# Optimization experiments

Measured on AMD Instinct MI355X. Metric: run time of the kernel, lower is better.

## Reference

```python
import jax, jax.numpy as jnp
import numpy as np

HEAD_SIZE = 64
EMB_SIZE = 1024
B, N = 4, 4096


def setup_inputs() -> dict:
    key = jax.random.key(0)
    kx, kk, kq, kv = jax.random.split(key, 4)
    x = jax.random.normal(kx, (B, N, EMB_SIZE), dtype=jnp.float32)
    # nn.Linear(emb, head, bias=False): weight [head, emb]; y = x @ W.T
    s = 1.0 / np.sqrt(EMB_SIZE)
    Wk = jax.random.uniform(kk, (HEAD_SIZE, EMB_SIZE), jnp.float32, -s, s)
    Wq = jax.random.uniform(kq, (HEAD_SIZE, EMB_SIZE), jnp.float32, -s, s)
    Wv = jax.random.uniform(kv, (HEAD_SIZE, EMB_SIZE), jnp.float32, -s, s)
    return {"x": x, "Wk": Wk, "Wq": Wq, "Wv": Wv}


def reference(x, Wk, Wq, Wv):
    # k, q, v: [B, N, H]
    k = jnp.einsum("bne,he->bnh", x, Wk)
    q = jnp.einsum("bne,he->bnh", x, Wq)
    v = jnp.einsum("bne,he->bnh", x, Wv)
    scale = HEAD_SIZE ** -0.5
    aff = jnp.einsum("bqh,bkh->bqk", q, k) * scale  # [B, N, N]
    aff = jax.nn.softmax(aff, axis=2)
    # dropout rate is 0.0 -> identity
    return jnp.einsum("bqk,bkh->bqh", aff, v)
```

## Files before the change

### kernel.cpp

```cpp
#include <hip/hip_runtime.h>

#define NB   4
#define SEQ  4096
#define EMB  1024
#define HS   64

typedef __attribute__((ext_vector_type(8))) short bf16x8;
typedef __attribute__((ext_vector_type(4))) float f32x4;

__device__ inline unsigned short f2bf(float f) {
  unsigned int u = __float_as_uint(f);
  u += 0x7fffu + ((u >> 16) & 1u);
  return (unsigned short)(u >> 16);
}
__device__ inline float bf2f(unsigned short h) {
  return __uint_as_float(((unsigned int)h) << 16);
}
__device__ inline int swzi64(int row, int c) {
  return row * 64 + ((c ^ (row & 7)) << 3);
}
__device__ inline int swzi32(int row, int c) {
  return row * 32 + ((c ^ ((row >> 1) & 3)) << 3);
}
__device__ inline int swzi128(int row, int c) {
  return row * 128 + ((c ^ (row & 7)) << 3);
}
__device__ inline void gld16(const unsigned short* g, unsigned short* l) {
  __builtin_amdgcn_global_load_lds(
      (const __attribute__((address_space(1))) void*)g,
      (__attribute__((address_space(3))) void*)l, 16, 0, 0);
}

__global__ __launch_bounds__(256) void wprep(
    const float* __restrict__ Wk, const float* __restrict__ Wq,
    const float* __restrict__ Wv,
    unsigned short* __restrict__ Wh, unsigned short* __restrict__ Wl) {
  int i = blockIdx.x * 256 + threadIdx.x;
  int e = i >> 8, c = i & 255;
  float4 v;
  float sc = 1.0f;
  if (e < 64)       { v = ((const float4*)Wq)[e * 256 + c];
                      sc = 0.18033688011112042f; }
  else if (e < 128)   v = ((const float4*)Wk)[(e - 64) * 256 + c];
  else                v = ((const float4*)Wv)[(e - 128) * 256 + c];
  v.x *= sc; v.y *= sc; v.z *= sc; v.w *= sc;
  ushort4 hv, lv;
  hv.x = f2bf(v.x); lv.x = f2bf(v.x - bf2f(hv.x));
  hv.y = f2bf(v.y); lv.y = f2bf(v.y - bf2f(hv.y));
  hv.z = f2bf(v.z); lv.z = f2bf(v.z - bf2f(hv.z));
  hv.w = f2bf(v.w); lv.w = f2bf(v.w - bf2f(hv.w));
  *(ushort4*)&Wh[i * 4] = hv;
  *(ushort4*)&Wl[i * 4] = lv;
}

#define XhSp(p) ((unsigned short*)(SM + (p) * 2048))
#define XlSp(p) ((unsigned short*)(SM + 4096 + (p) * 2048))
#define WhSp(p) ((unsigned short*)(SM + 8192 + (p) * 12288))
#define WlSp(p) ((unsigned short*)(SM + 32768 + (p) * 12288))

__global__ __launch_bounds__(256) void qkv_x1(
    const float* __restrict__ x,
    const unsigned short* __restrict__ Wh, const unsigned short* __restrict__ Wl,
    unsigned short* __restrict__ qh, unsigned short* __restrict__ ql,
    unsigned short* __restrict__ kh, unsigned short* __restrict__ kl,
    unsigned short* __restrict__ vt) {
  __shared__ __align__(16) unsigned char SM[57344];

  const int t  = threadIdx.x;
  const int l  = t & 63;
  const int li = l & 15;
  const int g  = l >> 4;
  const int w  = t >> 6;
  const int m0 = blockIdx.x * 32;
  const int b  = m0 >> 12;
  const int n0 = m0 & 4095;

  const int xrow = t >> 3;
  const float* xp = x + (m0 + xrow) * EMB + (t & 7) * 4;
  const int xaddr = xrow * 32 + ((((t & 7) >> 1) ^ ((xrow >> 1) & 3)) << 3)
                    + (t & 1) * 4;

  const int wconst = (l >> 2) * EMB + (((l & 3) ^ ((l >> 3) & 3)) << 3);

  f32x4 acc[2][3];
#pragma unroll
  for (int i = 0; i < 2; ++i)
#pragma unroll
    for (int j = 0; j < 3; ++j) acc[i][j] = (f32x4){0.f, 0.f, 0.f, 0.f};

  const int rA0 = li, rA1 = 16 + li;
  const int rB0 = 48 * w + li, rB1 = rB0 + 16, rB2 = rB0 + 32;

  auto issueW = [&](int s, int p) {
    const int ko = s * 32;
#pragma unroll
    for (int i = 0; i < 3; ++i) {
      const int seg = 3 * w + i;
      gld16(Wh + 16 * seg * EMB + wconst + ko, WhSp(p) + seg * 512);
      gld16(Wl + 16 * seg * EMB + wconst + ko, WlSp(p) + seg * 512);
    }
  };
  auto writeX = [&](float4 v, int p) {
    unsigned short h0 = f2bf(v.x), h1 = f2bf(v.y), h2 = f2bf(v.z), h3 = f2bf(v.w);
    unsigned short e0 = f2bf(v.x - bf2f(h0)), e1 = f2bf(v.y - bf2f(h1));
    unsigned short e2 = f2bf(v.z - bf2f(h2)), e3 = f2bf(v.w - bf2f(h3));
    int2 hv, lv;
    hv.x = (int)((unsigned)h0 | ((unsigned)h1 << 16));
    hv.y = (int)((unsigned)h2 | ((unsigned)h3 << 16));
    lv.x = (int)((unsigned)e0 | ((unsigned)e1 << 16));
    lv.y = (int)((unsigned)e2 | ((unsigned)e3 << 16));
    *(int2*)&XhSp(p)[xaddr] = hv;
    *(int2*)&XlSp(p)[xaddr] = lv;
  };

  float4 px = *(const float4*)xp;
  issueW(0, 0);
  writeX(px, 0);
  px = *(const float4*)(xp + 32);
  __syncthreads();

  for (int s = 0; s < 32; ++s) {
    const int p = s & 1;
    if (s < 31) {
      issueW(s + 1, p ^ 1);
      writeX(px, p ^ 1);
      if (s < 30) px = *(const float4*)(xp + (s + 2) * 32);
    }

    bf16x8 ah0 = *(const bf16x8*)&XhSp(p)[swzi32(rA0, g)];
    bf16x8 ah1 = *(const bf16x8*)&XhSp(p)[swzi32(rA1, g)];
    bf16x8 al0 = *(const bf16x8*)&XlSp(p)[swzi32(rA0, g)];
    bf16x8 al1 = *(const bf16x8*)&XlSp(p)[swzi32(rA1, g)];
    bf16x8 bh0 = *(const bf16x8*)&WhSp(p)[swzi32(rB0, g)];
    bf16x8 bh1 = *(const bf16x8*)&WhSp(p)[swzi32(rB1, g)];
    bf16x8 bh2 = *(const bf16x8*)&WhSp(p)[swzi32(rB2, g)];
    bf16x8 bl0 = *(const bf16x8*)&WlSp(p)[swzi32(rB0, g)];
    bf16x8 bl1 = *(const bf16x8*)&WlSp(p)[swzi32(rB1, g)];
    bf16x8 bl2 = *(const bf16x8*)&WlSp(p)[swzi32(rB2, g)];

    acc[0][0] = __builtin_amdgcn_mfma_f32_16x16x32_bf16(ah0, bh0, acc[0][0], 0,0,0);
    acc[0][0] = __builtin_amdgcn_mfma_f32_16x16x32_bf16(ah0, bl0, acc[0][0], 0,0,0);
    acc[0][0] = __builtin_amdgcn_mfma_f32_16x16x32_bf16(al0, bh0, acc[0][0], 0,0,0);
    acc[0][1] = __builtin_amdgcn_mfma_f32_16x16x32_bf16(ah0, bh1, acc[0][1], 0,0,0);
    acc[0][1] = __builtin_amdgcn_mfma_f32_16x16x32_bf16(ah0, bl1, acc[0][1], 0,0,0);
    acc[0][1] = __builtin_amdgcn_mfma_f32_16x16x32_bf16(al0, bh1, acc[0][1], 0,0,0);
    acc[0][2] = __builtin_amdgcn_mfma_f32_16x16x32_bf16(ah0, bh2, acc[0][2], 0,0,0);
    acc[0][2] = __builtin_amdgcn_mfma_f32_16x16x32_bf16(ah0, bl2, acc[0][2], 0,0,0);
    acc[0][2] = __builtin_amdgcn_mfma_f32_16x16x32_bf16(al0, bh2, acc[0][2], 0,0,0);
    acc[1][0] = __builtin_amdgcn_mfma_f32_16x16x32_bf16(ah1, bh0, acc[1][0], 0,0,0);
    acc[1][0] = __builtin_amdgcn_mfma_f32_16x16x32_bf16(ah1, bl0, acc[1][0], 0,0,0);
    acc[1][0] = __builtin_amdgcn_mfma_f32_16x16x32_bf16(al1, bh0, acc[1][0], 0,0,0);
    acc[1][1] = __builtin_amdgcn_mfma_f32_16x16x32_bf16(ah1, bh1, acc[1][1], 0,0,0);
    acc[1][1] = __builtin_amdgcn_mfma_f32_16x16x32_bf16(ah1, bl1, acc[1][1], 0,0,0);
    acc[1][1] = __builtin_amdgcn_mfma_f32_16x16x32_bf16(al1, bh1, acc[1][1], 0,0,0);
    acc[1][2] = __builtin_amdgcn_mfma_f32_16x16x32_bf16(ah1, bh2, acc[1][2], 0,0,0);
    acc[1][2] = __builtin_amdgcn_mfma_f32_16x16x32_bf16(ah1, bl2, acc[1][2], 0,0,0);
    acc[1][2] = __builtin_amdgcn_mfma_f32_16x16x32_bf16(al1, bh2, acc[1][2], 0,0,0);

    __syncthreads();
  }

#pragma unroll
  for (int i = 0; i < 2; ++i)
#pragma unroll
    for (int j = 0; j < 3; ++j) {
      const int H3 = 48 * w + 16 * j + li;
#pragma unroll
      for (int r = 0; r < 4; ++r) {
        const int mrow = 16 * i + 4 * g + r;
        const float vv = acc[i][j][r];
        if (H3 < 64) {
          const unsigned short hb = f2bf(vv);
          const int off = (b * SEQ + n0 + mrow) * HS + H3;
          qh[off] = hb; ql[off] = f2bf(vv - bf2f(hb));
        } else if (H3 < 128) {
          const unsigned short hb = f2bf(vv);
          const int off = (b * SEQ + n0 + mrow) * HS + (H3 - 64);
          kh[off] = hb; kl[off] = f2bf(vv - bf2f(hb));
        } else {
          vt[(b * HS + (H3 - 128)) * SEQ + n0 + mrow] = f2bf(vv);
        }
      }
    }
}

__global__ __launch_bounds__(512) void attn_mfma(
    const unsigned short* __restrict__ qh, const unsigned short* __restrict__ ql,
    const unsigned short* __restrict__ kh, const unsigned short* __restrict__ kl,
    const unsigned short* __restrict__ vt, float* __restrict__ out) {
  __shared__ __align__(16) unsigned char SM[69632];
  unsigned short* const KhS = (unsigned short*)SM;
  unsigned short* const KlS = (unsigned short*)(SM + 16384);
  unsigned short* const VtS = (unsigned short*)(SM + 32768);
  unsigned short* const PtS = (unsigned short*)(SM + 49152);

  const int t  = threadIdx.x;
  const int l  = t & 63;
  const int li = l & 15;
  const int g  = l >> 4;
  const int w  = t >> 6;
  const int qg = w & 1;
  const int ks = w >> 1;
  const int b  = blockIdx.y;
  const int q0 = blockIdx.x << 6;

  bf16x8 qfh[2][2], qfl[2][2];
#pragma unroll
  for (int qs = 0; qs < 2; ++qs) {
    const unsigned short* qrh = qh + (b * SEQ + q0 + 32 * qg + 16 * qs + li) * HS;
    const unsigned short* qrl = ql + (b * SEQ + q0 + 32 * qg + 16 * qs + li) * HS;
    qfh[qs][0] = *(const bf16x8*)&qrh[8 * g];
    qfh[qs][1] = *(const bf16x8*)&qrh[32 + 8 * g];
    qfl[qs][0] = *(const bf16x8*)&qrl[8 * g];
    qfl[qs][1] = *(const bf16x8*)&qrl[32 + 8 * g];
  }

  const int kconst = (l >> 3) * HS + (((l & 7) ^ (l >> 3)) << 3);
  const int rowl = l >> 4, slot = l & 15;
  const int vcE = rowl * SEQ + ((slot ^ rowl) << 3);
  const int vcO = rowl * SEQ + ((slot ^ (4 + rowl)) << 3);
  const unsigned short* khB = kh + b * SEQ * HS;
  const unsigned short* klB = kl + b * SEQ * HS;
  const unsigned short* vtB = vt + b * HS * SEQ;
  const int sA = 2 * w, sB = 2 * w + 1;

  f32x4 O[4][2];
#pragma unroll
  for (int ht = 0; ht < 4; ++ht) {
    O[ht][0] = (f32x4){0.f, 0.f, 0.f, 0.f};
    O[ht][1] = (f32x4){0.f, 0.f, 0.f, 0.f};
  }
  float lp0 = 0.f, lp1 = 0.f;
  unsigned short* const PtW = PtS + w * 1280;

  for (int it = 0; it < 32; ++it) {
    const int kt0 = it << 7;
    __syncthreads();
    gld16(khB + (kt0 + 8 * sA) * HS + kconst, KhS + sA * 512);
    gld16(khB + (kt0 + 8 * sB) * HS + kconst, KhS + sB * 512);
    gld16(klB + (kt0 + 8 * sA) * HS + kconst, KlS + sA * 512);
    gld16(klB + (kt0 + 8 * sB) * HS + kconst, KlS + sB * 512);
    gld16(vtB + 4 * sA * SEQ + kt0 + vcE, VtS + sA * 512);
    gld16(vtB + 4 * sB * SEQ + kt0 + vcO, VtS + sB * 512);
    __syncthreads();

    f32x4 S[2][2];
    S[0][0] = (f32x4){-32.f, -32.f, -32.f, -32.f};
    S[0][1] = (f32x4){-32.f, -32.f, -32.f, -32.f};
    S[1][0] = (f32x4){-32.f, -32.f, -32.f, -32.f};
    S[1][1] = (f32x4){-32.f, -32.f, -32.f, -32.f};
#pragma unroll
    for (int khf = 0; khf < 2; ++khf) {
      const int cc = 4 * khf + g;
#pragma unroll
      for (int kt = 0; kt < 2; ++kt) {
        const int row = 32 * ks + 16 * kt + li;
        bf16x8 akh = *(const bf16x8*)&KhS[swzi64(row, cc)];
        bf16x8 akl = *(const bf16x8*)&KlS[swzi64(row, cc)];
        S[kt][0] = __builtin_amdgcn_mfma_f32_16x16x32_bf16(akh, qfh[0][khf], S[kt][0], 0,0,0);
        S[kt][0] = __builtin_amdgcn_mfma_f32_16x16x32_bf16(akh, qfl[0][khf], S[kt][0], 0,0,0);
        S[kt][0] = __builtin_amdgcn_mfma_f32_16x16x32_bf16(akl, qfh[0][khf], S[kt][0], 0,0,0);
        S[kt][1] = __builtin_amdgcn_mfma_f32_16x16x32_bf16(akh, qfh[1][khf], S[kt][1], 0,0,0);
        S[kt][1] = __builtin_amdgcn_mfma_f32_16x16x32_bf16(akh, qfl[1][khf], S[kt][1], 0,0,0);
        S[kt][1] = __builtin_amdgcn_mfma_f32_16x16x32_bf16(akl, qfh[1][khf], S[kt][1], 0,0,0);
      }
    }

#pragma unroll
    for (int kt = 0; kt < 2; ++kt)
#pragma unroll
      for (int qs = 0; qs < 2; ++qs) {
        unsigned pu[4];
        float ls = 0.f;
#pragma unroll
        for (int r = 0; r < 4; ++r) {
          const float pe = exp2f(S[kt][qs][r]);
          pu[r] = __float_as_uint(pe);
          ls += __uint_as_float(pu[r] & 0xffff0000u);
        }
        if (qs == 0) lp0 += ls; else lp1 += ls;
        const unsigned p01 = __builtin_amdgcn_perm(pu[1], pu[0], 0x07060302u);
        const unsigned p23 = __builtin_amdgcn_perm(pu[3], pu[2], 0x07060302u);
        const int qrow = 16 * qs + li;
        const int c = 2 * kt + (g >> 1);
        const int addr = qrow * 40 + (((c ^ (qrow & 3))) << 3) + ((g & 1) << 2);
        int2 pv; pv.x = (int)p01; pv.y = (int)p23;
        *(int2*)&PtW[addr] = pv;
      }

    asm volatile("" ::: "memory");

    bf16x8 pb0 = *(const bf16x8*)&PtW[li * 40 + ((g ^ (li & 3)) << 3)];
    {
      const int r1 = 16 + li;
      bf16x8 pb1 = *(const bf16x8*)&PtW[r1 * 40 + ((g ^ (r1 & 3)) << 3)];
#pragma unroll
      for (int ht = 0; ht < 4; ++ht) {
        const int vrow = 16 * ht + li;
        bf16x8 va = *(const bf16x8*)&VtS[swzi128(vrow, 4 * ks + g)];
        O[ht][0] = __builtin_amdgcn_mfma_f32_16x16x32_bf16(va, pb0, O[ht][0], 0,0,0);
        O[ht][1] = __builtin_amdgcn_mfma_f32_16x16x32_bf16(va, pb1, O[ht][1], 0,0,0);
      }
    }
  }

  __syncthreads();

  lp0 += __shfl_xor(lp0, 16); lp0 += __shfl_xor(lp0, 32);
  lp1 += __shfl_xor(lp1, 16); lp1 += __shfl_xor(lp1, 32);

  float* const OTm = (float*)SM;
  float* const Lm  = (float*)(SM + 65536);
#pragma unroll
  for (int ht = 0; ht < 4; ++ht)
#pragma unroll
    for (int qs = 0; qs < 2; ++qs) {
      float4 o4;
      o4.x = O[ht][qs][0]; o4.y = O[ht][qs][1];
      o4.z = O[ht][qs][2]; o4.w = O[ht][qs][3];
      *(float4*)&OTm[w * 2048 + (16 * qs + li) * 64 + 16 * ht + 4 * g] = o4;
    }
  if (g == 0) { Lm[w * 32 + li] = lp0; Lm[w * 32 + 16 + li] = lp1; }
  __syncthreads();

  {
    const int q = t >> 3, h8 = (t & 7) << 3;
    const int qq = q & 31, qgf = q >> 5;
    float lF = 0.f;
    float4 a = {0.f, 0.f, 0.f, 0.f}, c4 = {0.f, 0.f, 0.f, 0.f};
#pragma unroll
    for (int k2 = 0; k2 < 4; ++k2) {
      const int ww = qgf + 2 * k2;
      lF += Lm[ww * 32 + qq];
      const float* Ob = OTm + ww * 2048 + qq * 64 + h8;
      float4 u = *(const float4*)Ob;
      float4 v = *(const float4*)(Ob + 4);
      a.x += u.x; a.y += u.y; a.z += u.z; a.w += u.w;
      c4.x += v.x; c4.y += v.y; c4.z += v.z; c4.w += v.w;
    }
    const float inv = 1.f / lF;
    a.x *= inv; a.y *= inv; a.z *= inv; a.w *= inv;
    c4.x *= inv; c4.y *= inv; c4.z *= inv; c4.w *= inv;
    float* op = out + (b * SEQ + q0 + q) * HS + h8;
    *(float4*)op = a;
    *(float4*)(op + 4) = c4;
  }
}

extern "C" void kernel_launch(void* const* d_in, const int* in_sizes, int n_in,
                              void* d_out, int out_size, void* d_ws,
                              size_t ws_size, hipStream_t stream) {
  const float* x  = (const float*)d_in[0];
  const float* Wk = (const float*)d_in[1];
  const float* Wq = (const float*)d_in[2];
  const float* Wv = (const float*)d_in[3];
  float* out = (float*)d_out;

  unsigned short* us = (unsigned short*)d_ws;
  unsigned short* qh = us + 0 * (1 << 20);
  unsigned short* ql = us + 1 * (1 << 20);
  unsigned short* kh = us + 2 * (1 << 20);
  unsigned short* kl = us + 3 * (1 << 20);
  unsigned short* vt = us + 4 * (1 << 20);
  unsigned short* Wh = us + 5 * (1 << 20);
  unsigned short* Wl = Wh + 192 * 1024;

  wprep<<<192, 256, 0, stream>>>(Wk, Wq, Wv, Wh, Wl);
  qkv_x1<<<512, 256, 0, stream>>>(x, Wh, Wl, qh, ql, kh, kl, vt);
  attn_mfma<<<dim3(64, NB), 512, 0, stream>>>(qh, ql, kh, kl, vt, out);
}
```

Before: 205.3 us.

## Double-buffer K/V LDS tiles and raise wave priority around MFMA blocks

Splits the K-high, K-low and V-transposed shared-memory tiles into two ping-pong buffers. The next key block's global-to-LDS loads are issued at the top of each iteration, before the current block's QK^T, softmax and PV work, so they overlap with compute. This also drops one of the two barriers per iteration. MFMA sections are wrapped in s_setprio(1)/s_setprio(0) so matrix-issuing waves get scheduling priority. In exchange, LDS per block grows to about 116 KB, which could limit co-resident blocks if more than one block were scheduled per CU.

```diff
diff --git a/kernel.cpp b/kernel.cpp
--- a/kernel.cpp
+++ b/kernel.cpp
@@ -188,11 +188,8 @@
     const unsigned short* __restrict__ qh, const unsigned short* __restrict__ ql,
     const unsigned short* __restrict__ kh, const unsigned short* __restrict__ kl,
     const unsigned short* __restrict__ vt, float* __restrict__ out) {
-  __shared__ __align__(16) unsigned char SM[69632];
-  unsigned short* const KhS = (unsigned short*)SM;
-  unsigned short* const KlS = (unsigned short*)(SM + 16384);
-  unsigned short* const VtS = (unsigned short*)(SM + 32768);
-  unsigned short* const PtS = (unsigned short*)(SM + 49152);
+  __shared__ __align__(16) unsigned char SM[118784];
+  unsigned short* const PtS = (unsigned short*)(SM + 98304);
 
   const int t  = threadIdx.x;
   const int l  = t & 63;
@@ -233,22 +230,36 @@
   float lp0 = 0.f, lp1 = 0.f;
   unsigned short* const PtW = PtS + w * 1280;
 
+  auto stage = [&](int it, int p) {
+    const int kt0 = it << 7;
+    unsigned short* const KhP = (unsigned short*)(SM + p * 16384);
+    unsigned short* const KlP = (unsigned short*)(SM + 32768 + p * 16384);
+    unsigned short* const VtP = (unsigned short*)(SM + 65536 + p * 16384);
+    gld16(khB + (kt0 + 8 * sA) * HS + kconst, KhP + sA * 512);
+    gld16(khB + (kt0 + 8 * sB) * HS + kconst, KhP + sB * 512);
+    gld16(klB + (kt0 + 8 * sA) * HS + kconst, KlP + sA * 512);
+    gld16(klB + (kt0 + 8 * sB) * HS + kconst, KlP + sB * 512);
+    gld16(vtB + 4 * sA * SEQ + kt0 + vcE, VtP + sA * 512);
+    gld16(vtB + 4 * sB * SEQ + kt0 + vcO, VtP + sB * 512);
+  };
+
+  stage(0, 0);
+  __syncthreads();
+
   for (int it = 0; it < 32; ++it) {
-    const int kt0 = it << 7;
-    __syncthreads();
-    gld16(khB + (kt0 + 8 * sA) * HS + kconst, KhS + sA * 512);
-    gld16(khB + (kt0 + 8 * sB) * HS + kconst, KhS + sB * 512);
-    gld16(klB + (kt0 + 8 * sA) * HS + kconst, KlS + sA * 512);
-    gld16(klB + (kt0 + 8 * sB) * HS + kconst, KlS + sB * 512);
-    gld16(vtB + 4 * sA * SEQ + kt0 + vcE, VtS + sA * 512);
-    gld16(vtB + 4 * sB * SEQ + kt0 + vcO, VtS + sB * 512);
-    __syncthreads();
+    const int p = it & 1;
+    if (it < 31) stage(it + 1, p ^ 1);
+
+    unsigned short* const KhS = (unsigned short*)(SM + p * 16384);
+    unsigned short* const KlS = (unsigned short*)(SM + 32768 + p * 16384);
+    unsigned short* const VtS = (unsigned short*)(SM + 65536 + p * 16384);
 
     f32x4 S[2][2];
     S[0][0] = (f32x4){-32.f, -32.f, -32.f, -32.f};
     S[0][1] = (f32x4){-32.f, -32.f, -32.f, -32.f};
     S[1][0] = (f32x4){-32.f, -32.f, -32.f, -32.f};
     S[1][1] = (f32x4){-32.f, -32.f, -32.f, -32.f};
+    __builtin_amdgcn_s_setprio(1);
 #pragma unroll
     for (int khf = 0; khf < 2; ++khf) {
       const int cc = 4 * khf + g;
@@ -265,6 +276,7 @@
         S[kt][1] = __builtin_amdgcn_mfma_f32_16x16x32_bf16(akl, qfh[1][khf], S[kt][1], 0,0,0);
       }
     }
+    __builtin_amdgcn_s_setprio(0);
 
 #pragma unroll
     for (int kt = 0; kt < 2; ++kt)
@@ -294,6 +306,7 @@
     {
       const int r1 = 16 + li;
       bf16x8 pb1 = *(const bf16x8*)&PtW[r1 * 40 + ((g ^ (r1 & 3)) << 3)];
+      __builtin_amdgcn_s_setprio(1);
 #pragma unroll
       for (int ht = 0; ht < 4; ++ht) {
         const int vrow = 16 * ht + li;
@@ -301,10 +314,12 @@
         O[ht][0] = __builtin_amdgcn_mfma_f32_16x16x32_bf16(va, pb0, O[ht][0], 0,0,0);
         O[ht][1] = __builtin_amdgcn_mfma_f32_16x16x32_bf16(va, pb1, O[ht][1], 0,0,0);
       }
-    }
-  }
-
-  __syncthreads();
+      __builtin_amdgcn_s_setprio(0);
+    }
+
+    __syncthreads();
+  }
+
 
   lp0 += __shfl_xor(lp0, 16); lp0 += __shfl_xor(lp0, 32);
   lp1 += __shfl_xor(lp1, 16); lp1 += __shfl_xor(lp1, 32);
```

Measured after the change: 188.6 us. 8.1% less time.
